# Performance work log

Hardware: AMD Instinct MI355X
Metric: run time of the kernel (lower is better)

## Reference

```python
import jax, jax.numpy as jnp
import numpy as np

# ---- ATSSPostProcessor config ----
PRE_NMS_THRESH = 0.05
PRE_NMS_TOP_N  = 400      # k candidates per image (pre_nms_top_n)
NMS_THRESH     = 0.4
POST_TOP_N     = 100      # fpn_post_nms_top_n
MIN_SIZE       = 0.0
NUM_ANGLE_BINS = 90
BBOX_W         = (10.0, 10.0, 5.0, 5.0)   # box_coder xywh weights; angle is passthrough (argmax-90 deg)
N, C, H, W     = 4, 15, 256, 256           # A=1 anchor per location
STRIDE, ANCHOR_SIZE = 8.0, 64.0
MAXV = 16                                   # vertex buffer for quad-quad clipping


def setup_inputs():
    key = jax.random.key(0)
    k1, k2, k3, k4 = jax.random.split(key, 4)
    box_cls = jax.random.normal(k1, (N, C, H, W), jnp.float32) - 2.0  # sigmoid ~0.12 avg -> plenty of candidates
    box_regression = jax.random.normal(k2, (N, 4, H, W), jnp.float32) * 0.5
    centerness = jax.random.normal(k3, (N, 1, H, W), jnp.float32)
    angle = jax.random.normal(k4, (N, NUM_ANGLE_BINS, H, W), jnp.float32)
    # xywha anchors on the stride-8 grid, row-major (H, W) to match permute_and_flatten ordering
    ys, xs = jnp.meshgrid(jnp.arange(H, dtype=jnp.float32), jnp.arange(W, dtype=jnp.float32), indexing='ij')
    cx = (xs.reshape(-1) + 0.5) * STRIDE
    cy = (ys.reshape(-1) + 0.5) * STRIDE
    wh = jnp.full((H * W,), ANCHOR_SIZE, jnp.float32)
    a0 = jnp.zeros((H * W,), jnp.float32)
    anchors = jnp.broadcast_to(jnp.stack([cx, cy, wh, wh, a0], -1), (N, H * W, 5))
    return {"box_cls": box_cls, "box_regression": box_regression, "centerness": centerness,
            "angle": angle, "anchors": jnp.asarray(anchors)}


def xywha_to_corners(b):
    # b [..., 5] (cx,cy,w,h,angle_deg) -> [..., 4, 2], CCW order
    cx, cy, w, h, a = b[..., 0], b[..., 1], b[..., 2], b[..., 3], b[..., 4]
    t = a * (jnp.pi / 180.0)
    c, s = jnp.cos(t), jnp.sin(t)
    ox = jnp.asarray([1., -1., -1., 1.], b.dtype) * (w[..., None] * 0.5)
    oy = jnp.asarray([1., 1., -1., -1.], b.dtype) * (h[..., None] * 0.5)
    x = cx[..., None] + ox * c[..., None] - oy * s[..., None]
    y = cy[..., None] + ox * s[..., None] + oy * c[..., None]
    return jnp.stack([x, y], -1)


def _clip_edge(poly, n, p1, p2):
    # Sutherland-Hodgman: clip CCW polygon (poly[:n]) against half-plane left of p1->p2
    e = p2 - p1
    d = e[0] * (poly[:, 1] - p1[1]) - e[1] * (poly[:, 0] - p1[0])  # >= 0 is inside
    def body(i, carry):
        out, m = carry
        j = jnp.where(i == n - 1, 0, i + 1)
        cur, nxt, dc, dn = poly[i], poly[j], d[i], d[j]
        denom = dc - dn
        denom = jnp.where(jnp.abs(denom) < 1e-8, 1e-8, denom)
        ip = cur + (dc / denom) * (nxt - cur)
        act = i < n
        a1 = act & (dc >= 0)
        out = out.at[m].set(jnp.where(a1, cur, out[m]))
        m = m + a1.astype(jnp.int32)
        a2 = act & ((dc >= 0) != (dn >= 0))
        out = out.at[m].set(jnp.where(a2, ip, out[m]))
        m = m + a2.astype(jnp.int32)
        return out, m
    return jax.lax.fori_loop(0, 8, body, (jnp.zeros_like(poly), jnp.int32(0)))


def _quad_inter_area(c1, c2):
    # intersection area of two CCW quads via polygon clipping + shoelace
    poly = jnp.zeros((MAXV, 2), c1.dtype).at[:4].set(c1)
    n = jnp.int32(4)
    def edge(e, carry):
        poly, n = carry
        return _clip_edge(poly, n, c2[e], c2[(e + 1) % 4])
    poly, n = jax.lax.fori_loop(0, 4, edge, (poly, n))
    idx = jnp.arange(MAXV)
    j = jnp.where(idx == n - 1, 0, idx + 1)
    mask = idx < n
    terms = poly[:, 0] * poly[j, 1] - poly[j, 0] * poly[:, 1]
    return 0.5 * jnp.abs(jnp.sum(jnp.where(mask, terms, 0.0)))


def _riou_matrix(boxes):                        # [k,5] -> [k,k] rotated IoU
    corners = xywha_to_corners(boxes)           # [k,4,2]
    areas = boxes[:, 2] * boxes[:, 3]
    def one(ci, ai):
        def two(cj, aj):
            inter = _quad_inter_area(ci, cj)
            return inter / (ai + aj - inter + 1e-7)
        return jax.vmap(two)(corners, areas)
    return jax.vmap(one)(corners, areas)


@jax.jit
def _forward(box_cls, box_regression, centerness, angle, anchors):
    n, c, h, w = box_cls.shape
    K, k = h * w, PRE_NMS_TOP_N
    # permute_and_flatten + activations
    cls = jax.nn.sigmoid(box_cls).transpose(0, 2, 3, 1).reshape(n, K, c)
    reg = box_regression.transpose(0, 2, 3, 1).reshape(n, K, 4)
    ctr = jax.nn.sigmoid(centerness).reshape(n, K)
    ang = jax.nn.softmax(angle.transpose(0, 2, 3, 1).reshape(n, K, NUM_ANGLE_BINS), axis=-1)
    # pre-nms threshold on raw sigmoid cls, topk on cls*centerness
    cand = cls > PRE_NMS_THRESH
    comb = cls * ctr[:, :, None]
    flat = jnp.where(cand, comb, -1.0).reshape(n, K * c)
    topv, topi = jax.lax.top_k(flat, k)          # sorted descending
    valid = topv > 0.0                           # emulates per_pre_nms_top_n clamp
    loc = topi // c
    labels = topi % c + 1
    reg_s = jnp.take_along_axis(reg, loc[..., None], axis=1)       # [n,k,4]
    anc_s = jnp.take_along_axis(anchors, loc[..., None], axis=1)   # [n,k,5]
    ang_s = jnp.take_along_axis(ang, loc[..., None], axis=1)       # [n,k,90]
    pred_angle = jnp.argmax(ang_s, axis=-1).astype(reg_s.dtype) - 90.0
    # box_coder.decode (xywh deltas, angle passthrough)
    wx, wy, ww, wh = BBOX_W
    dx, dy = reg_s[..., 0] / wx, reg_s[..., 1] / wy
    dw = jnp.clip(reg_s[..., 2] / ww, -10.0, 4.0)
    dh = jnp.clip(reg_s[..., 3] / wh, -10.0, 4.0)
    acx, acy, aw, ah = anc_s[..., 0], anc_s[..., 1], anc_s[..., 2], anc_s[..., 3]
    boxes = jnp.stack([dx * aw + acx, dy * ah + acy,
                       aw * jnp.exp(dw), ah * jnp.exp(dh), pred_angle], -1)
    valid = valid & (boxes[..., 2] >= MIN_SIZE) & (boxes[..., 3] >= MIN_SIZE)
    scores = jnp.where(valid, jnp.sqrt(jnp.maximum(topv, 0.0)), 0.0)
    # class-aware rotated NMS (boxlist_ml_rnms): IoU only within same class
    iou = jax.lax.stop_gradient(jax.vmap(_riou_matrix)(boxes))     # [n,k,k]
    same = labels[:, :, None] == labels[:, None, :]
    iou = jnp.where(same, iou, 0.0)
    idxs = jnp.arange(k)
    def body(i, keep):
        sup = keep[:, i][:, None] & (iou[:, i, :] > NMS_THRESH) & (idxs[None, :] > i)
        return keep & ~sup
    keep = jax.lax.fori_loop(0, k, body, valid)
    # keep top fpn_post_nms_top_n by score
    fscore = jnp.where(keep, scores, -1.0)
    fv, fi = jax.lax.top_k(fscore, POST_TOP_N)
    fvalid = fv > 0.0
    fboxes = jnp.take_along_axis(boxes, fi[..., None], axis=1)
    flabels = jnp.take_along_axis(labels, fi, axis=1)
    corners = xywha_to_corners(fboxes).reshape(n, POST_TOP_N, 8)   # convert('xyxyxyxy')
    out = jnp.concatenate([corners,
                           jnp.maximum(fv, 0.0)[..., None],
                           flabels.astype(corners.dtype)[..., None],
                           fvalid.astype(corners.dtype)[..., None]], -1)
    return out * fvalid[..., None].astype(out.dtype)   # [N, POST_TOP_N, 11]


def reference(box_cls, box_regression, centerness, angle, anchors):
    return _forward(box_cls, box_regression, centerness, angle, anchors)
```

## Files before the change

### kernel.cpp

```cpp
#include <hip/hip_runtime.h>
#include <math.h>

#define NIMG 4
#define NCLS 15
#define HW 65536
#define NANG 90
#define KTOP 400
#define POSTN 100
#define NBINS 4096
#define CAP 4096

#define HIST_OFF   0
#define CNT_OFF    65536
#define SUPT_OFF   65600
#define ZERO_BYTES 165952
#define CAND_OFF   165952
#define SKEY_OFF   297024
#define COR_OFF    309824
#define AREA_OFF   361024
#define LAB_OFF    367424
#define SC_OFF     373824
#define VAL_OFF    380224
#define CCX_OFF    386624
#define CCY_OFF    393024
#define CRAD_OFF   399424

__device__ __forceinline__ float sigmoidf(float x) {
    return 1.0f / (1.0f + expf(-x));
}

__global__ __launch_bounds__(256)
void k_hist(const float* __restrict__ cls, const float* __restrict__ ctr,
            int* __restrict__ hist) {
    __shared__ int sh[NBINS];
    const int n = blockIdx.y;
    const int p2 = (blockIdx.x * 256 + threadIdx.x) * 2;
    for (int b = threadIdx.x; b < NBINS; b += 256) sh[b] = 0;
    __syncthreads();
    float2 cv2 = *(const float2*)(ctr + n * HW + p2);
    float cv[2] = {sigmoidf(cv2.x), sigmoidf(cv2.y)};
    for (int j = 0; j < NCLS; ++j) {
        float2 s2 = *(const float2*)(cls + (size_t)(n * NCLS + j) * HW + p2);
        float sv[2] = {s2.x, s2.y};
#pragma unroll
        for (int e = 0; e < 2; ++e) {
            float s = sigmoidf(sv[e]);
            if (s > 0.05f) {
                float comb = s * cv[e];
                int b = (int)(comb * 4096.0f);
                b = b < 0 ? 0 : (b > NBINS - 1 ? NBINS - 1 : b);
                atomicAdd(&sh[b], 1);
            }
        }
    }
    __syncthreads();
    for (int b = threadIdx.x; b < NBINS; b += 256) {
        int v = sh[b];
        if (v) atomicAdd(&hist[n * NBINS + b], v);
    }
}

__global__ __launch_bounds__(256)
void k_collect(const float* __restrict__ cls, const float* __restrict__ ctr,
               const int* __restrict__ hist, int* __restrict__ cnt,
               unsigned long long* __restrict__ cand) {
    const int n = blockIdx.y;
    __shared__ int part[256];
    __shared__ int s_t;
    {
        const int* hb = hist + n * NBINS;
        int s = 0;
        int base = threadIdx.x * 16;
        for (int b = 0; b < 16; ++b) s += hb[base + b];
        part[threadIdx.x] = s;
        if (threadIdx.x == 0) s_t = 0;
        __syncthreads();
        for (int off = 1; off < 256; off <<= 1) {
            int v = part[threadIdx.x] +
                    ((threadIdx.x + off < 256) ? part[threadIdx.x + off] : 0);
            __syncthreads();
            part[threadIdx.x] = v;
            __syncthreads();
        }
        int sg = threadIdx.x;
        int suf = part[sg];
        int above = (sg == 255) ? 0 : part[sg + 1];
        if (suf >= KTOP && above < KTOP) {
            int a2 = above, t = sg * 16;
            for (int b = sg * 16 + 15; b >= sg * 16; --b) {
                a2 += hb[b];
                if (a2 >= KTOP) { t = b; break; }
            }
            s_t = t;
        }
        __syncthreads();
    }
    const int t = s_t;
    const int p2 = (blockIdx.x * 256 + threadIdx.x) * 2;
    float2 cv2 = *(const float2*)(ctr + n * HW + p2);
    float cv[2] = {sigmoidf(cv2.x), sigmoidf(cv2.y)};
    for (int j = 0; j < NCLS; ++j) {
        float2 s2 = *(const float2*)(cls + (size_t)(n * NCLS + j) * HW + p2);
        float sv[2] = {s2.x, s2.y};
#pragma unroll
        for (int e = 0; e < 2; ++e) {
            float s = sigmoidf(sv[e]);
            if (s > 0.05f) {
                float comb = s * cv[e];
                int b = (int)(comb * 4096.0f);
                b = b < 0 ? 0 : (b > NBINS - 1 ? NBINS - 1 : b);
                if (b >= t) {
                    int pos = atomicAdd(&cnt[n], 1);
                    if (pos < CAP) {
                        unsigned int fb  = __float_as_uint(comb);
                        unsigned int idx = (unsigned int)((p2 + e) * NCLS + j);
                        cand[n * CAP + pos] =
                            ((unsigned long long)fb << 32) | (unsigned long long)(~idx);
                    }
                }
            }
        }
    }
}

__global__ __launch_bounds__(256)
void k_select(const unsigned long long* __restrict__ cand, const int* __restrict__ cnt,
              unsigned long long* __restrict__ skey) {
    const int n = blockIdx.x;
    __shared__ unsigned long long key[CAP];
    int c = cnt[n];
    if (c > CAP) c = CAP;
    int S = 512;
    while (S < c) S <<= 1;
    for (int t = threadIdx.x; t < S; t += 256)
        key[t] = (t < c) ? cand[n * CAP + t] : 0ULL;
    __syncthreads();
    for (int k = 2; k <= S; k <<= 1) {
        for (int j = k >> 1; j > 0; j >>= 1) {
            for (int i = threadIdx.x; i < S; i += 256) {
                int l = i ^ j;
                if (l > i) {
                    unsigned long long a = key[i], b = key[l];
                    bool up = ((i & k) == 0);
                    if ((a > b) == up) { key[i] = b; key[l] = a; }
                }
            }
            __syncthreads();
        }
    }
    for (int r = threadIdx.x; r < KTOP; r += 256)
        skey[n * KTOP + r] = key[S - 1 - r];
}

__global__ __launch_bounds__(64)
void k_decode(const unsigned long long* __restrict__ skey,
              const float* __restrict__ reg, const float* __restrict__ ang,
              const float* __restrict__ anchors,
              float* __restrict__ cor, float* __restrict__ area, int* __restrict__ lab,
              float* __restrict__ sc, int* __restrict__ val,
              float* __restrict__ ccx, float* __restrict__ ccy, float* __restrict__ crad) {
#pragma clang fp contract(off)
    const int r = blockIdx.x;
    const int n = blockIdx.y;
    const int l = threadIdx.x;
    const int base = n * KTOP + r;
    unsigned long long kk = skey[base];
    if (kk == 0ULL) {
        if (l == 0) {
            val[base] = 0; sc[base] = 0.0f; lab[base] = 0; area[base] = 0.0f;
            ccx[base] = 0.0f; ccy[base] = 0.0f; crad[base] = 0.0f;
            for (int q = 0; q < 8; ++q) cor[base * 8 + q] = 0.0f;
        }
        return;
    }
    unsigned int idx = ~((unsigned int)kk);
    int loc = (int)(idx / 15u);
    const float* ap = ang + ((size_t)n * NANG) * HW + loc;
    float bv = -INFINITY; int bb = 1000;
    for (int b = l; b < NANG; b += 64) {
        float v = ap[(size_t)b * HW];
        if (v > bv) { bv = v; bb = b; }
    }
    for (int off = 32; off > 0; off >>= 1) {
        float ov = __shfl_down(bv, off);
        int   ob = __shfl_down(bb, off);
        if (ov > bv || (ov == bv && ob < bb)) { bv = ov; bb = ob; }
    }
    if (l == 0) {
        int cl = (int)(idx % 15u);
        float topv = __uint_as_float((unsigned int)(kk >> 32));
        const float* rp = reg + ((size_t)n * 4) * HW + loc;
        float dx = rp[0] / 10.0f;
        float dy = rp[HW] / 10.0f;
        float dw = rp[2 * (size_t)HW] / 5.0f;
        float dh = rp[3 * (size_t)HW] / 5.0f;
        dw = fminf(fmaxf(dw, -10.0f), 4.0f);
        dh = fminf(fmaxf(dh, -10.0f), 4.0f);
        const float* an = anchors + ((size_t)n * HW + loc) * 5;
        float acx = an[0], acy = an[1], aw = an[2], ah = an[3];
        float bcx = dx * aw + acx;
        float bcy = dy * ah + acy;
        float bw = aw * expf(dw);
        float bh = ah * expf(dh);
        float pa = (float)bb - 90.0f;
        float th = pa * (float)0.017453292519943295;
        float cth = cosf(th), sth = sinf(th);
        float hw2 = bw * 0.5f, hh2 = bh * 0.5f;
        const float oxs[4] = {1.0f, -1.0f, -1.0f, 1.0f};
        const float oys[4] = {1.0f, 1.0f, -1.0f, -1.0f};
        for (int q = 0; q < 4; ++q) {
            float ox = oxs[q] * hw2, oy = oys[q] * hh2;
            cor[base * 8 + 2 * q]     = bcx + ox * cth - oy * sth;
            cor[base * 8 + 2 * q + 1] = bcy + ox * sth + oy * cth;
        }
        val[base] = 1;
        sc[base] = sqrtf(topv);
        lab[base] = cl + 1;
        area[base] = bw * bh;
        ccx[base] = bcx; ccy[base] = bcy;
        crad[base] = 0.5f * sqrtf(bw * bw + bh * bh);
    }
}

__device__ __forceinline__ float arr_get8(const float* a, int idx) {
    float r = a[0];
#pragma unroll
    for (int s = 1; s < 8; ++s) r = (s == idx) ? a[s] : r;
    return r;
}
__device__ __forceinline__ void arr_set8(float* a, int idx, float v) {
#pragma unroll
    for (int s = 0; s < 8; ++s) a[s] = (s == idx) ? v : a[s];
}

__device__ float quad_inter_area(const float* c1x, const float* c1y,
                                 const float* c2x, const float* c2y) {
#pragma clang fp contract(off)
    float px[8], py[8], qx[8], qy[8];
    int n = 4;
#pragma unroll
    for (int i = 0; i < 8; ++i) { px[i] = (i < 4) ? c1x[i] : 0.0f;
                                  py[i] = (i < 4) ? c1y[i] : 0.0f;
                                  qx[i] = 0.0f; qy[i] = 0.0f; }
#pragma unroll
    for (int e = 0; e < 4; ++e) {
        float p1x = c2x[e], p1y = c2y[e];
        int e2 = (e + 1) & 3;
        float ex = c2x[e2] - p1x, ey = c2y[e2] - p1y;
        int m = 0;
#pragma unroll
        for (int i = 0; i < 8; ++i) {
            if (i < n) {
                int j = (i == n - 1) ? 0 : i + 1;
                float cxi = px[i], cyi = py[i];
                float cxj = arr_get8(px, j), cyj = arr_get8(py, j);
                float dc = ex * (cyi - p1y) - ey * (cxi - p1x);
                float dn = ex * (cyj - p1y) - ey * (cxj - p1x);
                bool ic = (dc >= 0.0f), in2 = (dn >= 0.0f);
                if (ic) { arr_set8(qx, m, cxi); arr_set8(qy, m, cyi); ++m; }
                if (ic != in2) {
                    float denom = dc - dn;
                    if (fabsf(denom) < 1e-8f) denom = 1e-8f;
                    float tp = dc / denom;
                    arr_set8(qx, m, cxi + tp * (cxj - cxi));
                    arr_set8(qy, m, cyi + tp * (cyj - cyi));
                    ++m;
                }
            }
        }
        n = m;
        if (n == 0) return 0.0f;
#pragma unroll
        for (int i = 0; i < 8; ++i) { px[i] = qx[i]; py[i] = qy[i]; }
    }
    float ssum = 0.0f;
#pragma unroll
    for (int i = 0; i < 8; ++i) {
        if (i < n) {
            int j = (i == n - 1) ? 0 : i + 1;
            ssum += px[i] * arr_get8(py, j) - arr_get8(px, j) * py[i];
        }
    }
    return 0.5f * fabsf(ssum);
}

__global__ __launch_bounds__(256)
void k_pairs(const float* __restrict__ cor, const float* __restrict__ area,
             const int* __restrict__ lab,
             const float* __restrict__ ccx, const float* __restrict__ ccy,
             const float* __restrict__ crad,
             unsigned long long* __restrict__ supT) {
#pragma clang fp contract(off)
    const int n = blockIdx.y;
    const int p = blockIdx.x * 256 + threadIdx.x;
    if (p >= KTOP * KTOP) return;
    const int i = p / KTOP;
    const int j = p - i * KTOP;
    if (j <= i) return;
    const int base = n * KTOP;
    const int li = lab[base + i];
    if (li == 0 || lab[base + j] != li) return;
    float dx = ccx[base + i] - ccx[base + j];
    float dy = ccy[base + i] - ccy[base + j];
    float rr = crad[base + i] + crad[base + j];
    if (dx * dx + dy * dy > rr * rr) return;
    float cix[4], ciy[4], cjx[4], cjy[4];
    for (int q = 0; q < 4; ++q) {
        cix[q] = cor[(base + i) * 8 + 2 * q]; ciy[q] = cor[(base + i) * 8 + 2 * q + 1];
        cjx[q] = cor[(base + j) * 8 + 2 * q]; cjy[q] = cor[(base + j) * 8 + 2 * q + 1];
    }
    float inter = quad_inter_area(cix, ciy, cjx, cjy);
    float iou = inter / (area[base + i] + area[base + j] - inter + 1e-7f);
    if (iou > 0.4f) {
        atomicOr(&supT[((size_t)(n * 7 + (j >> 6)) * 7 + (i >> 6)) * 64 + (j & 63)],
                 1ULL << (i & 63));
    }
}

__global__ __launch_bounds__(64)
void k_nms_out(const unsigned long long* __restrict__ supT,
               const int* __restrict__ val,
               const float* __restrict__ cor, const float* __restrict__ sc,
               const int* __restrict__ lab, float* __restrict__ out) {
    const int n = blockIdx.x;
    const int l = threadIdx.x;
    unsigned removed = 0;
#pragma unroll
    for (int t = 0; t < 7; ++t) {
        int r = 64 * t + l;
        int v = (r < KTOP) ? val[n * KTOP + r] : 0;
        if (!v) removed |= (1u << t);
    }
    unsigned long long cm[7][7];
#pragma unroll
    for (int t = 0; t < 7; ++t)
#pragma unroll
        for (int rb = 0; rb < 7; ++rb)
            cm[t][rb] = supT[((size_t)(n * 7 + t) * 7 + rb) * 64 + l];
#pragma unroll
    for (int rb = 0; rb < 7; ++rb) {
        const int lim = (rb == 6) ? (KTOP - 384) : 64;
        for (int ib = 0; ib < lim; ++ib) {
            unsigned rm = (unsigned)__builtin_amdgcn_readlane((int)removed, ib);
            if (!((rm >> rb) & 1u)) {
                removed |= ((unsigned)((cm[0][rb] >> ib) & 1ULL));
                removed |= ((unsigned)((cm[1][rb] >> ib) & 1ULL)) << 1;
                removed |= ((unsigned)((cm[2][rb] >> ib) & 1ULL)) << 2;
                removed |= ((unsigned)((cm[3][rb] >> ib) & 1ULL)) << 3;
                removed |= ((unsigned)((cm[4][rb] >> ib) & 1ULL)) << 4;
                removed |= ((unsigned)((cm[5][rb] >> ib) & 1ULL)) << 5;
                removed |= ((unsigned)((cm[6][rb] >> ib) & 1ULL)) << 6;
            }
        }
    }
    __shared__ int order[POSTN];
    int rank = 0;
#pragma unroll
    for (int t = 0; t < 7; ++t) {
        bool kb = !((removed >> t) & 1u) && (64 * t + l < KTOP);
        unsigned long long m = __ballot(kb);
        int my = rank + __popcll(m & ((1ULL << l) - 1ULL));
        if (kb && my < POSTN) order[my] = 64 * t + l;
        rank += __popcll(m);
    }
    int kcnt = rank < POSTN ? rank : POSTN;
    __syncthreads();
    for (int e = l; e < POSTN * 11; e += 64) {
        int r = e / 11, c = e - r * 11;
        float v = 0.0f;
        if (r < kcnt) {
            int i = order[r];
            int b = n * KTOP + i;
            if (c < 8)       v = cor[b * 8 + c];
            else if (c == 8) v = sc[b];
            else if (c == 9) v = (float)lab[b];
            else             v = 1.0f;
        }
        out[(n * POSTN + r) * 11 + c] = v;
    }
}

extern "C" void kernel_launch(void* const* d_in, const int* in_sizes, int n_in,
                              void* d_out, int out_size, void* d_ws, size_t ws_size,
                              hipStream_t stream) {
    const float* box_cls = (const float*)d_in[0];
    const float* box_reg = (const float*)d_in[1];
    const float* ctr     = (const float*)d_in[2];
    const float* ang     = (const float*)d_in[3];
    const float* anchors = (const float*)d_in[4];
    float* out = (float*)d_out;
    char* ws = (char*)d_ws;

    int* hist = (int*)(ws + HIST_OFF);
    int* cnt  = (int*)(ws + CNT_OFF);
    unsigned long long* supT = (unsigned long long*)(ws + SUPT_OFF);
    unsigned long long* cand = (unsigned long long*)(ws + CAND_OFF);
    unsigned long long* skey = (unsigned long long*)(ws + SKEY_OFF);
    float* cor  = (float*)(ws + COR_OFF);
    float* area = (float*)(ws + AREA_OFF);
    int* lab    = (int*)(ws + LAB_OFF);
    float* sc   = (float*)(ws + SC_OFF);
    int* val    = (int*)(ws + VAL_OFF);
    float* ccx  = (float*)(ws + CCX_OFF);
    float* ccy  = (float*)(ws + CCY_OFF);
    float* crad = (float*)(ws + CRAD_OFF);

    hipMemsetAsync(d_ws, 0, ZERO_BYTES, stream);
    k_hist   <<<dim3(HW / 512, NIMG), 256, 0, stream>>>(box_cls, ctr, hist);
    k_collect<<<dim3(HW / 512, NIMG), 256, 0, stream>>>(box_cls, ctr, hist, cnt, cand);
    k_select <<<NIMG, 256, 0, stream>>>(cand, cnt, skey);
    k_decode <<<dim3(KTOP, NIMG), 64, 0, stream>>>(skey, box_reg, ang, anchors,
                                                   cor, area, lab, sc, val, ccx, ccy, crad);
    k_pairs  <<<dim3((KTOP * KTOP + 255) / 256, NIMG), 256, 0, stream>>>(
                 cor, area, lab, ccx, ccy, crad, supT);
    k_nms_out<<<NIMG, 64, 0, stream>>>(supT, val, cor, sc, lab, out);
}
```

Baseline: 247.9 us.

## Fuse sort and decode into one 1024-thread kernel, preload class scores

Merges the bitonic top-k sort and the per-candidate box decode into a single kernel with 1024 threads per image. Two threads split each candidate's 90-bin angle argmax, and the same kernel zeroes the suppression matrix, which shrinks the memset. The histogram and collect kernels now issue all 15 class loads up front, and in collect those loads start before the threshold scan so their latency overlaps it. This drops one launch and the skey round trip, but decode now runs on only 4 blocks with a serial 45-step strided angle loop per thread.

```diff
diff --git a/kernel.cpp b/kernel.cpp
--- a/kernel.cpp
+++ b/kernel.cpp
@@ -12,18 +12,17 @@
 
 #define HIST_OFF   0
 #define CNT_OFF    65536
+#define ZERO_BYTES 65600
 #define SUPT_OFF   65600
-#define ZERO_BYTES 165952
 #define CAND_OFF   165952
-#define SKEY_OFF   297024
-#define COR_OFF    309824
-#define AREA_OFF   361024
-#define LAB_OFF    367424
-#define SC_OFF     373824
-#define VAL_OFF    380224
-#define CCX_OFF    386624
-#define CCY_OFF    393024
-#define CRAD_OFF   399424
+#define COR_OFF    297024
+#define AREA_OFF   348224
+#define LAB_OFF    354624
+#define SC_OFF     361024
+#define VAL_OFF    367424
+#define CCX_OFF    373824
+#define CCY_OFF    380224
+#define CRAD_OFF   386624
 
 __device__ __forceinline__ float sigmoidf(float x) {
     return 1.0f / (1.0f + expf(-x));
@@ -38,13 +37,17 @@
     for (int b = threadIdx.x; b < NBINS; b += 256) sh[b] = 0;
     __syncthreads();
     float2 cv2 = *(const float2*)(ctr + n * HW + p2);
+    float2 sv[NCLS];
+#pragma unroll
+    for (int j = 0; j < NCLS; ++j)
+        sv[j] = *(const float2*)(cls + (size_t)(n * NCLS + j) * HW + p2);
     float cv[2] = {sigmoidf(cv2.x), sigmoidf(cv2.y)};
+#pragma unroll
     for (int j = 0; j < NCLS; ++j) {
-        float2 s2 = *(const float2*)(cls + (size_t)(n * NCLS + j) * HW + p2);
-        float sv[2] = {s2.x, s2.y};
+        float v2[2] = {sv[j].x, sv[j].y};
 #pragma unroll
         for (int e = 0; e < 2; ++e) {
-            float s = sigmoidf(sv[e]);
+            float s = sigmoidf(v2[e]);
             if (s > 0.05f) {
                 float comb = s * cv[e];
                 int b = (int)(comb * 4096.0f);
@@ -65,6 +68,12 @@
                const int* __restrict__ hist, int* __restrict__ cnt,
                unsigned long long* __restrict__ cand) {
     const int n = blockIdx.y;
+    const int p2 = (blockIdx.x * 256 + threadIdx.x) * 2;
+    float2 cv2 = *(const float2*)(ctr + n * HW + p2);
+    float2 sv[NCLS];
+#pragma unroll
+    for (int j = 0; j < NCLS; ++j)
+        sv[j] = *(const float2*)(cls + (size_t)(n * NCLS + j) * HW + p2);
     __shared__ int part[256];
     __shared__ int s_t;
     {
@@ -96,15 +105,13 @@
         __syncthreads();
     }
     const int t = s_t;
-    const int p2 = (blockIdx.x * 256 + threadIdx.x) * 2;
-    float2 cv2 = *(const float2*)(ctr + n * HW + p2);
     float cv[2] = {sigmoidf(cv2.x), sigmoidf(cv2.y)};
+#pragma unroll
     for (int j = 0; j < NCLS; ++j) {
-        float2 s2 = *(const float2*)(cls + (size_t)(n * NCLS + j) * HW + p2);
-        float sv[2] = {s2.x, s2.y};
+        float v2[2] = {sv[j].x, sv[j].y};
 #pragma unroll
         for (int e = 0; e < 2; ++e) {
-            float s = sigmoidf(sv[e]);
+            float s = sigmoidf(v2[e]);
             if (s > 0.05f) {
                 float comb = s * cv[e];
                 int b = (int)(comb * 4096.0f);
@@ -123,102 +130,101 @@
     }
 }
 
-__global__ __launch_bounds__(256)
-void k_select(const unsigned long long* __restrict__ cand, const int* __restrict__ cnt,
-              unsigned long long* __restrict__ skey) {
+__global__ __launch_bounds__(1024)
+void k_sortdec(const unsigned long long* __restrict__ cand, const int* __restrict__ cnt,
+               const float* __restrict__ reg, const float* __restrict__ ang,
+               const float* __restrict__ anchors,
+               unsigned long long* __restrict__ supT,
+               float* __restrict__ cor, float* __restrict__ area, int* __restrict__ lab,
+               float* __restrict__ sc, int* __restrict__ val,
+               float* __restrict__ ccx, float* __restrict__ ccy, float* __restrict__ crad) {
+#pragma clang fp contract(off)
     const int n = blockIdx.x;
-    __shared__ unsigned long long key[CAP];
+    const int tid = threadIdx.x;
+    __shared__ unsigned long long keys[CAP];
+
+    for (int i = tid; i < 7 * 7 * 64; i += 1024)
+        supT[(size_t)n * (7 * 7 * 64) + i] = 0ULL;
+
     int c = cnt[n];
     if (c > CAP) c = CAP;
     int S = 512;
     while (S < c) S <<= 1;
-    for (int t = threadIdx.x; t < S; t += 256)
-        key[t] = (t < c) ? cand[n * CAP + t] : 0ULL;
+    for (int i = tid; i < S; i += 1024)
+        keys[i] = (i < c) ? cand[n * CAP + i] : 0ULL;
     __syncthreads();
     for (int k = 2; k <= S; k <<= 1) {
         for (int j = k >> 1; j > 0; j >>= 1) {
-            for (int i = threadIdx.x; i < S; i += 256) {
+            for (int i = tid; i < S; i += 1024) {
                 int l = i ^ j;
                 if (l > i) {
-                    unsigned long long a = key[i], b = key[l];
+                    unsigned long long a = keys[i], b = keys[l];
                     bool up = ((i & k) == 0);
-                    if ((a > b) == up) { key[i] = b; key[l] = a; }
+                    if ((a > b) == up) { keys[i] = b; keys[l] = a; }
                 }
             }
             __syncthreads();
         }
     }
-    for (int r = threadIdx.x; r < KTOP; r += 256)
-        skey[n * KTOP + r] = key[S - 1 - r];
-}
-
-__global__ __launch_bounds__(64)
-void k_decode(const unsigned long long* __restrict__ skey,
-              const float* __restrict__ reg, const float* __restrict__ ang,
-              const float* __restrict__ anchors,
-              float* __restrict__ cor, float* __restrict__ area, int* __restrict__ lab,
-              float* __restrict__ sc, int* __restrict__ val,
-              float* __restrict__ ccx, float* __restrict__ ccy, float* __restrict__ crad) {
-#pragma clang fp contract(off)
-    const int r = blockIdx.x;
-    const int n = blockIdx.y;
-    const int l = threadIdx.x;
-    const int base = n * KTOP + r;
-    unsigned long long kk = skey[base];
-    if (kk == 0ULL) {
-        if (l == 0) {
-            val[base] = 0; sc[base] = 0.0f; lab[base] = 0; area[base] = 0.0f;
-            ccx[base] = 0.0f; ccy[base] = 0.0f; crad[base] = 0.0f;
-            for (int q = 0; q < 8; ++q) cor[base * 8 + q] = 0.0f;
-        }
-        return;
-    }
-    unsigned int idx = ~((unsigned int)kk);
-    int loc = (int)(idx / 15u);
-    const float* ap = ang + ((size_t)n * NANG) * HW + loc;
-    float bv = -INFINITY; int bb = 1000;
-    for (int b = l; b < NANG; b += 64) {
-        float v = ap[(size_t)b * HW];
-        if (v > bv) { bv = v; bb = b; }
-    }
-    for (int off = 32; off > 0; off >>= 1) {
-        float ov = __shfl_down(bv, off);
-        int   ob = __shfl_down(bb, off);
-        if (ov > bv || (ov == bv && ob < bb)) { bv = ov; bb = ob; }
-    }
-    if (l == 0) {
-        int cl = (int)(idx % 15u);
-        float topv = __uint_as_float((unsigned int)(kk >> 32));
-        const float* rp = reg + ((size_t)n * 4) * HW + loc;
-        float dx = rp[0] / 10.0f;
-        float dy = rp[HW] / 10.0f;
-        float dw = rp[2 * (size_t)HW] / 5.0f;
-        float dh = rp[3 * (size_t)HW] / 5.0f;
-        dw = fminf(fmaxf(dw, -10.0f), 4.0f);
-        dh = fminf(fmaxf(dh, -10.0f), 4.0f);
-        const float* an = anchors + ((size_t)n * HW + loc) * 5;
-        float acx = an[0], acy = an[1], aw = an[2], ah = an[3];
-        float bcx = dx * aw + acx;
-        float bcy = dy * ah + acy;
-        float bw = aw * expf(dw);
-        float bh = ah * expf(dh);
-        float pa = (float)bb - 90.0f;
-        float th = pa * (float)0.017453292519943295;
-        float cth = cosf(th), sth = sinf(th);
-        float hw2 = bw * 0.5f, hh2 = bh * 0.5f;
-        const float oxs[4] = {1.0f, -1.0f, -1.0f, 1.0f};
-        const float oys[4] = {1.0f, 1.0f, -1.0f, -1.0f};
-        for (int q = 0; q < 4; ++q) {
-            float ox = oxs[q] * hw2, oy = oys[q] * hh2;
-            cor[base * 8 + 2 * q]     = bcx + ox * cth - oy * sth;
-            cor[base * 8 + 2 * q + 1] = bcy + ox * sth + oy * cth;
-        }
-        val[base] = 1;
-        sc[base] = sqrtf(topv);
-        lab[base] = cl + 1;
-        area[base] = bw * bh;
-        ccx[base] = bcx; ccy[base] = bcy;
-        crad[base] = 0.5f * sqrtf(bw * bw + bh * bh);
+
+    if (tid < 2 * KTOP) {
+        const int r = tid >> 1, half = tid & 1;
+        const int base = n * KTOP + r;
+        unsigned long long kk = keys[S - 1 - r];
+        if (kk == 0ULL) {
+            if (half == 0) {
+                val[base] = 0; sc[base] = 0.0f; lab[base] = 0; area[base] = 0.0f;
+                ccx[base] = 0.0f; ccy[base] = 0.0f; crad[base] = 0.0f;
+                for (int q = 0; q < 8; ++q) cor[base * 8 + q] = 0.0f;
+            }
+        } else {
+            unsigned int idx = ~((unsigned int)kk);
+            int loc = (int)(idx / 15u);
+            const float* ap = ang + ((size_t)n * NANG) * HW + loc;
+            float bv = -INFINITY; int bb = 1000;
+            for (int k2 = 0; k2 < 45; ++k2) {
+                int b = half * 45 + k2;
+                float v = ap[(size_t)b * HW];
+                if (v > bv) { bv = v; bb = b; }
+            }
+            float ov = __shfl_xor(bv, 1);
+            int   ob = __shfl_xor(bb, 1);
+            if (ov > bv || (ov == bv && ob < bb)) { bv = ov; bb = ob; }
+            if (half == 0) {
+                int cl = (int)(idx % 15u);
+                float topv = __uint_as_float((unsigned int)(kk >> 32));
+                const float* rp = reg + ((size_t)n * 4) * HW + loc;
+                float dx = rp[0] / 10.0f;
+                float dy = rp[HW] / 10.0f;
+                float dw = rp[2 * (size_t)HW] / 5.0f;
+                float dh = rp[3 * (size_t)HW] / 5.0f;
+                dw = fminf(fmaxf(dw, -10.0f), 4.0f);
+                dh = fminf(fmaxf(dh, -10.0f), 4.0f);
+                const float* an = anchors + ((size_t)n * HW + loc) * 5;
+                float acx = an[0], acy = an[1], aw = an[2], ah = an[3];
+                float bcx = dx * aw + acx;
+                float bcy = dy * ah + acy;
+                float bw = aw * expf(dw);
+                float bh = ah * expf(dh);
+                float pa = (float)bb - 90.0f;
+                float th = pa * (float)0.017453292519943295;
+                float cth = cosf(th), sth = sinf(th);
+                float hw2 = bw * 0.5f, hh2 = bh * 0.5f;
+                const float oxs[4] = {1.0f, -1.0f, -1.0f, 1.0f};
+                const float oys[4] = {1.0f, 1.0f, -1.0f, -1.0f};
+                for (int q = 0; q < 4; ++q) {
+                    float ox = oxs[q] * hw2, oy = oys[q] * hh2;
+                    cor[base * 8 + 2 * q]     = bcx + ox * cth - oy * sth;
+                    cor[base * 8 + 2 * q + 1] = bcy + ox * sth + oy * cth;
+                }
+                val[base] = 1;
+                sc[base] = sqrtf(topv);
+                lab[base] = cl + 1;
+                area[base] = bw * bh;
+                ccx[base] = bcx; ccy[base] = bcy;
+                crad[base] = 0.5f * sqrtf(bw * bw + bh * bh);
+            }
+        }
     }
 }
 
@@ -395,7 +401,6 @@
     int* cnt  = (int*)(ws + CNT_OFF);
     unsigned long long* supT = (unsigned long long*)(ws + SUPT_OFF);
     unsigned long long* cand = (unsigned long long*)(ws + CAND_OFF);
-    unsigned long long* skey = (unsigned long long*)(ws + SKEY_OFF);
     float* cor  = (float*)(ws + COR_OFF);
     float* area = (float*)(ws + AREA_OFF);
     int* lab    = (int*)(ws + LAB_OFF);
@@ -408,9 +413,8 @@
     hipMemsetAsync(d_ws, 0, ZERO_BYTES, stream);
     k_hist   <<<dim3(HW / 512, NIMG), 256, 0, stream>>>(box_cls, ctr, hist);
     k_collect<<<dim3(HW / 512, NIMG), 256, 0, stream>>>(box_cls, ctr, hist, cnt, cand);
-    k_select <<<NIMG, 256, 0, stream>>>(cand, cnt, skey);
-    k_decode <<<dim3(KTOP, NIMG), 64, 0, stream>>>(skey, box_reg, ang, anchors,
-                                                   cor, area, lab, sc, val, ccx, ccy, crad);
+    k_sortdec<<<NIMG, 1024, 0, stream>>>(cand, cnt, box_reg, ang, anchors, supT,
+                                         cor, area, lab, sc, val, ccx, ccy, crad);
     k_pairs  <<<dim3((KTOP * KTOP + 255) / 256, NIMG), 256, 0, stream>>>(
                  cor, area, lab, ccx, ccy, crad, supT);
     k_nms_out<<<NIMG, 64, 0, stream>>>(supT, val, cor, sc, lab, out);
```

Result: slower. 322.2 us (+30.0%).
